# Kernel tuning notes

Measured on AMD Instinct MI355X. Metric: run time of the kernel, lower is better.

## Reference

```python
import jax, jax.numpy as jnp
import numpy as np

B, C, H, W = 32, 512, 64, 64
NBCLASS = 17


def setup_inputs() -> dict:
    key = jax.random.key(0)
    k1, k2 = jax.random.split(key, 2)
    x = jax.random.normal(k1, (B, C, H, W), dtype=jnp.float32)
    # 1x1 conv == linear over channels: weight (nbclass, C), bias (nbclass,)
    w_class = jax.random.normal(k2, (NBCLASS, C), dtype=jnp.float32) * 0.02
    b_class = jnp.zeros((NBCLASS,), dtype=jnp.float32)
    return {"x": x, "w_class": w_class, "b_class": b_class}


def reference(x, w_class, b_class):
    # x: (B, C, H, W); w_class: (K, C); b_class: (K,)
    Bx, Cx, Hx, Wx = x.shape
    # g = convclass(adaptive_avg_pool(x)) flattened -> (B, K)
    g = jnp.mean(x, axis=(2, 3)) @ w_class.T + b_class
    # cam = convclass(x) -> (B, K, H, W)
    cam = jnp.einsum('kc,bchw->bkhw', w_class, x) + b_class[None, :, None, None]
    # sf = mean_{h,w} sigmoid(cam)[:,k] * x[:,c]  -> (B, K, C)
    # (fused form of the original repeat/broadcast-multiply-mean)
    sf = jnp.einsum('bkhw,bchw->bkc', jax.nn.sigmoid(cam), x) / (Hx * Wx)
    return (g, sf)
```

## Files before the change

### kernel.cpp

```cpp
#include <hip/hip_runtime.h>
#include <cmath>

#define BATCH 32
#define CCH 512
#define HW 4096
#define KCL 17

typedef __attribute__((ext_vector_type(8))) short short8;
typedef __attribute__((ext_vector_type(16))) float f32x16;
typedef __attribute__((ext_vector_type(4))) float f32x4;

__device__ __forceinline__ unsigned pack_bf16(float a, float b) {
  unsigned ua = (__float_as_uint(a) + 0x8000u) >> 16;
  unsigned ub = (__float_as_uint(b) + 0x8000u) & 0xFFFF0000u;
  return ua | ub;
}
__device__ __forceinline__ f32x4 ntload4(const float* p) {
  return __builtin_nontemporal_load(reinterpret_cast<const f32x4*>(p));
}

#define WT_OFF 0
#define WT_BYTES (CCH * 20 * 4)
#define SIG_OFF WT_BYTES
#define SIG_BYTES ((size_t)BATCH * 32 * HW * 2)
#define XBF_OFF (SIG_OFF + SIG_BYTES)
#define XBF_BYTES ((size_t)BATCH * CCH * HW * 2)
#define WS_NEED (XBF_OFF + XBF_BYTES)

__global__ void k0_setup(const float* __restrict__ w, float* __restrict__ wT,
                         float* __restrict__ out_g) {
  int c = threadIdx.x;
  #pragma unroll
  for (int k = 0; k < 20; ++k) wT[c * 20 + k] = (k < KCL) ? w[k * CCH + c] : 0.f;
  if (c < BATCH * KCL) out_g[c] = 0.f;
  if (c < BATCH * KCL - 512) out_g[512 + c] = 0.f;
}

__global__ __launch_bounds__(512)
void k12_cam_sig(const float* __restrict__ x, const float* __restrict__ wT,
                 const float* __restrict__ bias, float* __restrict__ out_g,
                 unsigned short* __restrict__ xbf, unsigned short* __restrict__ sig) {
  extern __shared__ float R[];
  const int t = threadIdx.x;
  const int slab = __builtin_amdgcn_readfirstlane(t >> 7);
  const int pxg = t & 127;
  const int b = blockIdx.x >> 3;
  const int slice = blockIdx.x & 7;
  const int px = slice * 512 + pxg * 4;
  const float* xp = x + ((size_t)(b * CCH + slab * 128)) * HW + px;
  unsigned short* xbp = xbf + ((size_t)(b * CCH + slab * 128)) * HW + px;

  float cam[KCL][4];
  #pragma unroll
  for (int k = 0; k < KCL; ++k)
    #pragma unroll
    for (int i = 0; i < 4; ++i) cam[k][i] = 0.f;

  f32x4 v0[4], v1[4];
  #pragma unroll
  for (int j = 0; j < 4; ++j) v0[j] = ntload4(xp + (size_t)j * HW);

  #pragma unroll 1
  for (int gp = 0; gp < 16; ++gp) {
    const int c0 = gp * 8;
    #pragma unroll
    for (int j = 0; j < 4; ++j) v1[j] = ntload4(xp + (size_t)(c0 + 4 + j) * HW);
    #pragma unroll
    for (int j = 0; j < 4; ++j) {
      const f32x4 v = v0[j];
      const float* wr = wT + (slab * 128 + c0 + j) * 20;
      #pragma unroll
      for (int k = 0; k < KCL; ++k) {
        cam[k][0] = fmaf(wr[k], v.x, cam[k][0]);
        cam[k][1] = fmaf(wr[k], v.y, cam[k][1]);
        cam[k][2] = fmaf(wr[k], v.z, cam[k][2]);
        cam[k][3] = fmaf(wr[k], v.w, cam[k][3]);
      }
      *reinterpret_cast<uint2*>(xbp + (size_t)(c0 + j) * HW) =
          make_uint2(pack_bf16(v.x, v.y), pack_bf16(v.z, v.w));
    }
    if (gp < 15) {
      #pragma unroll
      for (int j = 0; j < 4; ++j) v0[j] = ntload4(xp + (size_t)(c0 + 8 + j) * HW);
    }
    #pragma unroll
    for (int j = 0; j < 4; ++j) {
      const f32x4 v = v1[j];
      const float* wr = wT + (slab * 128 + c0 + 4 + j) * 20;
      #pragma unroll
      for (int k = 0; k < KCL; ++k) {
        cam[k][0] = fmaf(wr[k], v.x, cam[k][0]);
        cam[k][1] = fmaf(wr[k], v.y, cam[k][1]);
        cam[k][2] = fmaf(wr[k], v.z, cam[k][2]);
        cam[k][3] = fmaf(wr[k], v.w, cam[k][3]);
      }
      *reinterpret_cast<uint2*>(xbp + (size_t)(c0 + 4 + j) * HW) =
          make_uint2(pack_bf16(v.x, v.y), pack_bf16(v.z, v.w));
    }
  }

  if (slab >= 2) {
    float* Rb = R + (slab - 2) * (KCL * 512);
    #pragma unroll
    for (int k = 0; k < KCL; ++k)
      *reinterpret_cast<float4*>(Rb + k * 512 + pxg * 4) =
          make_float4(cam[k][0], cam[k][1], cam[k][2], cam[k][3]);
  }
  __syncthreads();
  if (slab < 2) {
    const float* Rb = R + slab * (KCL * 512);
    #pragma unroll
    for (int k = 0; k < KCL; ++k) {
      const float4 r = *reinterpret_cast<const float4*>(Rb + k * 512 + pxg * 4);
      cam[k][0] += r.x; cam[k][1] += r.y; cam[k][2] += r.z; cam[k][3] += r.w;
    }
  }
  __syncthreads();
  if (slab == 1) {
    #pragma unroll
    for (int k = 0; k < KCL; ++k)
      *reinterpret_cast<float4*>(R + k * 512 + pxg * 4) =
          make_float4(cam[k][0], cam[k][1], cam[k][2], cam[k][3]);
  }
  __syncthreads();
  if (slab == 0) {
    const float inv = 1.f / 4096.f;
    const int lane = t & 63;
    #pragma unroll
    for (int k = 0; k < KCL; ++k) {
      const float4 r = *reinterpret_cast<const float4*>(R + k * 512 + pxg * 4);
      const float bk = bias[k];
      float c0 = cam[k][0] + r.x + bk;
      float c1 = cam[k][1] + r.y + bk;
      float c2 = cam[k][2] + r.z + bk;
      float c3 = cam[k][3] + r.w + bk;
      unsigned u0 = pack_bf16(1.f / (1.f + __expf(-c0)), 1.f / (1.f + __expf(-c1)));
      unsigned u1 = pack_bf16(1.f / (1.f + __expf(-c2)), 1.f / (1.f + __expf(-c3)));
      *reinterpret_cast<uint2*>(sig + ((size_t)(b * 32 + k)) * HW + px) = make_uint2(u0, u1);
      float gk = c0 + c1 + c2 + c3;
      #pragma unroll
      for (int o = 1; o < 64; o <<= 1) gk += __shfl_xor(gk, o, 64);
      if (lane == 0) atomicAdd(out_g + b * KCL + k, gk * inv);
    }
  }
}

__global__ __launch_bounds__(512, 2)
void k3_sf(const unsigned short* __restrict__ xbf, const unsigned short* __restrict__ sig,
           float* __restrict__ out_sf) {
  __shared__ float P[8 * 1024];
  const int p = blockIdx.x;
  const int lid = (p & 7) * 64 + (p >> 3);
  const int b = lid >> 4;
  const int chs = lid & 15;
  const int t = threadIdx.x;
  const int lane = t & 63;
  const int wv = __builtin_amdgcn_readfirstlane(t >> 6);
  const int m = lane & 31;
  const int h = lane >> 5;

  const unsigned short* ap = xbf + ((size_t)(b * CCH + chs * 32 + m)) * HW;
  const unsigned short* bp = sig + ((size_t)(b * 32 + m)) * HW;

  f32x16 acc;
  #pragma unroll
  for (int i = 0; i < 16; ++i) acc[i] = 0.f;

  const int obase = (wv * 64 + h) * 8;
  #pragma unroll 4
  for (int i = 0; i < 32; ++i) {
    const int o = obase + i * 16;
    const short8 a = *reinterpret_cast<const short8*>(ap + o);
    const short8 bb = *reinterpret_cast<const short8*>(bp + o);
    acc = __builtin_amdgcn_mfma_f32_32x32x16_bf16(a, bb, acc, 0, 0, 0);
  }

  #pragma unroll
  for (int r = 0; r < 16; ++r) {
    const int chr = (r & 3) + 8 * (r >> 2) + 4 * h;
    P[wv * 1024 + m * 32 + chr] = acc[r];
  }
  __syncthreads();
  const float inv = 1.f / 4096.f;
  {
    float s = 0.f;
    #pragma unroll
    for (int w8 = 0; w8 < 8; ++w8) s += P[w8 * 1024 + t];
    const int n = t >> 5, ch = t & 31;
    out_sf[((size_t)b * KCL + n) * CCH + chs * 32 + ch] = s * inv;
    if (t < 32) {
      float s2 = 0.f;
      #pragma unroll
      for (int w8 = 0; w8 < 8; ++w8) s2 += P[w8 * 1024 + 512 + t];
      out_sf[((size_t)b * KCL + 16) * CCH + chs * 32 + t] = s2 * inv;
    }
  }
}

extern "C" void kernel_launch(void* const* d_in, const int* in_sizes, int n_in,
                              void* d_out, int out_size, void* d_ws, size_t ws_size,
                              hipStream_t stream) {
  const float* x = (const float*)d_in[0];
  const float* w = (const float*)d_in[1];
  const float* bias = (const float*)d_in[2];
  float* out = (float*)d_out;
  float* outg = out;
  float* outsf = out + BATCH * KCL;

  char* ws = (char*)d_ws;
  float* wT = (float*)(ws + WT_OFF);
  unsigned short* sig = (unsigned short*)(ws + SIG_OFF);
  unsigned short* xbf = (unsigned short*)(ws + XBF_OFF);

  k0_setup<<<1, 512, 0, stream>>>(w, wT, outg);

  const int k12_lds = 2 * KCL * 512 * 4;
  hipFuncSetAttribute((const void*)k12_cam_sig,
                      hipFuncAttributeMaxDynamicSharedMemorySize, k12_lds);
  k12_cam_sig<<<BATCH * 8, 512, k12_lds, stream>>>(x, wT, bias, outg, xbf, sig);

  k3_sf<<<BATCH * 16, 512, 0, stream>>>(xbf, sig, outsf);
}
```

Baseline: 117.8 us.

## Split channels into eight slabs with eight pixels per thread in cam kernel

The cam/sigmoid kernel now gives each wave a 64-channel slab and has each thread cover 8 pixels instead of 4. Each weight load is reused across twice as many FMAs, and the bf16 stores widen to 16 bytes. The cross-slab reduction becomes a three-level tree through LDS, which is doubled to 4 slabs worth. The cost is twice the accumulator registers (136 floats), a 1-block-per-CU launch bound, and fewer memory loads in flight per thread relative to compute, which risks register pressure and lower occupancy.

```diff
diff --git a/kernel.cpp b/kernel.cpp
--- a/kernel.cpp
+++ b/kernel.cpp
@@ -27,6 +27,8 @@
 #define XBF_BYTES ((size_t)BATCH * CCH * HW * 2)
 #define WS_NEED (XBF_OFF + XBF_BYTES)
 
+#define K12_LDS (4 * KCL * 512 * 4)
+
 __global__ void k0_setup(const float* __restrict__ w, float* __restrict__ wT,
                          float* __restrict__ out_g) {
   int c = threadIdx.x;
@@ -36,111 +38,173 @@
   if (c < BATCH * KCL - 512) out_g[512 + c] = 0.f;
 }
 
-__global__ __launch_bounds__(512)
+__global__ __launch_bounds__(512, 1)
 void k12_cam_sig(const float* __restrict__ x, const float* __restrict__ wT,
                  const float* __restrict__ bias, float* __restrict__ out_g,
                  unsigned short* __restrict__ xbf, unsigned short* __restrict__ sig) {
   extern __shared__ float R[];
   const int t = threadIdx.x;
-  const int slab = __builtin_amdgcn_readfirstlane(t >> 7);
-  const int pxg = t & 127;
+  const int slab = __builtin_amdgcn_readfirstlane(t >> 6);
+  const int pxg = t & 63;
   const int b = blockIdx.x >> 3;
   const int slice = blockIdx.x & 7;
-  const int px = slice * 512 + pxg * 4;
-  const float* xp = x + ((size_t)(b * CCH + slab * 128)) * HW + px;
-  unsigned short* xbp = xbf + ((size_t)(b * CCH + slab * 128)) * HW + px;
-
-  float cam[KCL][4];
+  const int px = slice * 512 + pxg * 8;
+  const float* xp = x + ((size_t)(b * CCH + slab * 64)) * HW + px;
+  unsigned short* xbp = xbf + ((size_t)(b * CCH + slab * 64)) * HW + px;
+
+  float cam[KCL][8];
   #pragma unroll
   for (int k = 0; k < KCL; ++k)
     #pragma unroll
-    for (int i = 0; i < 4; ++i) cam[k][i] = 0.f;
-
-  f32x4 v0[4], v1[4];
-  #pragma unroll
-  for (int j = 0; j < 4; ++j) v0[j] = ntload4(xp + (size_t)j * HW);
+    for (int i = 0; i < 8; ++i) cam[k][i] = 0.f;
+
+  f32x4 v0[2][2], v1[2][2];
+  #pragma unroll
+  for (int j = 0; j < 2; ++j) {
+    v0[j][0] = ntload4(xp + (size_t)j * HW);
+    v0[j][1] = ntload4(xp + (size_t)j * HW + 4);
+  }
 
   #pragma unroll 1
   for (int gp = 0; gp < 16; ++gp) {
-    const int c0 = gp * 8;
-    #pragma unroll
-    for (int j = 0; j < 4; ++j) v1[j] = ntload4(xp + (size_t)(c0 + 4 + j) * HW);
-    #pragma unroll
-    for (int j = 0; j < 4; ++j) {
-      const f32x4 v = v0[j];
-      const float* wr = wT + (slab * 128 + c0 + j) * 20;
+    const int c0 = gp * 4;
+    #pragma unroll
+    for (int j = 0; j < 2; ++j) {
+      v1[j][0] = ntload4(xp + (size_t)(c0 + 2 + j) * HW);
+      v1[j][1] = ntload4(xp + (size_t)(c0 + 2 + j) * HW + 4);
+    }
+    #pragma unroll
+    for (int j = 0; j < 2; ++j) {
+      const f32x4 a = v0[j][0], q = v0[j][1];
+      const float* wr = wT + (slab * 64 + c0 + j) * 20;
       #pragma unroll
       for (int k = 0; k < KCL; ++k) {
-        cam[k][0] = fmaf(wr[k], v.x, cam[k][0]);
-        cam[k][1] = fmaf(wr[k], v.y, cam[k][1]);
-        cam[k][2] = fmaf(wr[k], v.z, cam[k][2]);
-        cam[k][3] = fmaf(wr[k], v.w, cam[k][3]);
+        const float wk = wr[k];
+        cam[k][0] = fmaf(wk, a.x, cam[k][0]);
+        cam[k][1] = fmaf(wk, a.y, cam[k][1]);
+        cam[k][2] = fmaf(wk, a.z, cam[k][2]);
+        cam[k][3] = fmaf(wk, a.w, cam[k][3]);
+        cam[k][4] = fmaf(wk, q.x, cam[k][4]);
+        cam[k][5] = fmaf(wk, q.y, cam[k][5]);
+        cam[k][6] = fmaf(wk, q.z, cam[k][6]);
+        cam[k][7] = fmaf(wk, q.w, cam[k][7]);
       }
-      *reinterpret_cast<uint2*>(xbp + (size_t)(c0 + j) * HW) =
-          make_uint2(pack_bf16(v.x, v.y), pack_bf16(v.z, v.w));
+      uint4 u;
+      u.x = pack_bf16(a.x, a.y);
+      u.y = pack_bf16(a.z, a.w);
+      u.z = pack_bf16(q.x, q.y);
+      u.w = pack_bf16(q.z, q.w);
+      *reinterpret_cast<uint4*>(xbp + (size_t)(c0 + j) * HW) = u;
     }
     if (gp < 15) {
       #pragma unroll
-      for (int j = 0; j < 4; ++j) v0[j] = ntload4(xp + (size_t)(c0 + 8 + j) * HW);
-    }
-    #pragma unroll
-    for (int j = 0; j < 4; ++j) {
-      const f32x4 v = v1[j];
-      const float* wr = wT + (slab * 128 + c0 + 4 + j) * 20;
+      for (int j = 0; j < 2; ++j) {
+        v0[j][0] = ntload4(xp + (size_t)(c0 + 4 + j) * HW);
+        v0[j][1] = ntload4(xp + (size_t)(c0 + 4 + j) * HW + 4);
+      }
+    }
+    #pragma unroll
+    for (int j = 0; j < 2; ++j) {
+      const f32x4 a = v1[j][0], q = v1[j][1];
+      const float* wr = wT + (slab * 64 + c0 + 2 + j) * 20;
       #pragma unroll
       for (int k = 0; k < KCL; ++k) {
-        cam[k][0] = fmaf(wr[k], v.x, cam[k][0]);
-        cam[k][1] = fmaf(wr[k], v.y, cam[k][1]);
-        cam[k][2] = fmaf(wr[k], v.z, cam[k][2]);
-        cam[k][3] = fmaf(wr[k], v.w, cam[k][3]);
+        const float wk = wr[k];
+        cam[k][0] = fmaf(wk, a.x, cam[k][0]);
+        cam[k][1] = fmaf(wk, a.y, cam[k][1]);
+        cam[k][2] = fmaf(wk, a.z, cam[k][2]);
+        cam[k][3] = fmaf(wk, a.w, cam[k][3]);
+        cam[k][4] = fmaf(wk, q.x, cam[k][4]);
+        cam[k][5] = fmaf(wk, q.y, cam[k][5]);
+        cam[k][6] = fmaf(wk, q.z, cam[k][6]);
+        cam[k][7] = fmaf(wk, q.w, cam[k][7]);
       }
-      *reinterpret_cast<uint2*>(xbp + (size_t)(c0 + 4 + j) * HW) =
-          make_uint2(pack_bf16(v.x, v.y), pack_bf16(v.z, v.w));
-    }
-  }
-
-  if (slab >= 2) {
+      uint4 u;
+      u.x = pack_bf16(a.x, a.y);
+      u.y = pack_bf16(a.z, a.w);
+      u.z = pack_bf16(q.x, q.y);
+      u.w = pack_bf16(q.z, q.w);
+      *reinterpret_cast<uint4*>(xbp + (size_t)(c0 + 2 + j) * HW) = u;
+    }
+  }
+
+  const int base = pxg * 8;
+  if (slab >= 4) {
+    float* Rb = R + (slab - 4) * (KCL * 512);
+    #pragma unroll
+    for (int k = 0; k < KCL; ++k) {
+      *reinterpret_cast<float4*>(Rb + k * 512 + base) =
+          make_float4(cam[k][0], cam[k][1], cam[k][2], cam[k][3]);
+      *reinterpret_cast<float4*>(Rb + k * 512 + base + 4) =
+          make_float4(cam[k][4], cam[k][5], cam[k][6], cam[k][7]);
+    }
+  }
+  __syncthreads();
+  if (slab < 4) {
+    const float* Rb = R + slab * (KCL * 512);
+    #pragma unroll
+    for (int k = 0; k < KCL; ++k) {
+      const float4 r0 = *reinterpret_cast<const float4*>(Rb + k * 512 + base);
+      const float4 r1 = *reinterpret_cast<const float4*>(Rb + k * 512 + base + 4);
+      cam[k][0] += r0.x; cam[k][1] += r0.y; cam[k][2] += r0.z; cam[k][3] += r0.w;
+      cam[k][4] += r1.x; cam[k][5] += r1.y; cam[k][6] += r1.z; cam[k][7] += r1.w;
+    }
+  }
+  __syncthreads();
+  if (slab == 2 || slab == 3) {
     float* Rb = R + (slab - 2) * (KCL * 512);
     #pragma unroll
-    for (int k = 0; k < KCL; ++k)
-      *reinterpret_cast<float4*>(Rb + k * 512 + pxg * 4) =
+    for (int k = 0; k < KCL; ++k) {
+      *reinterpret_cast<float4*>(Rb + k * 512 + base) =
           make_float4(cam[k][0], cam[k][1], cam[k][2], cam[k][3]);
+      *reinterpret_cast<float4*>(Rb + k * 512 + base + 4) =
+          make_float4(cam[k][4], cam[k][5], cam[k][6], cam[k][7]);
+    }
   }
   __syncthreads();
   if (slab < 2) {
     const float* Rb = R + slab * (KCL * 512);
     #pragma unroll
     for (int k = 0; k < KCL; ++k) {
-      const float4 r = *reinterpret_cast<const float4*>(Rb + k * 512 + pxg * 4);
-      cam[k][0] += r.x; cam[k][1] += r.y; cam[k][2] += r.z; cam[k][3] += r.w;
+      const float4 r0 = *reinterpret_cast<const float4*>(Rb + k * 512 + base);
+      const float4 r1 = *reinterpret_cast<const float4*>(Rb + k * 512 + base + 4);
+      cam[k][0] += r0.x; cam[k][1] += r0.y; cam[k][2] += r0.z; cam[k][3] += r0.w;
+      cam[k][4] += r1.x; cam[k][5] += r1.y; cam[k][6] += r1.z; cam[k][7] += r1.w;
     }
   }
   __syncthreads();
   if (slab == 1) {
     #pragma unroll
-    for (int k = 0; k < KCL; ++k)
-      *reinterpret_cast<float4*>(R + k * 512 + pxg * 4) =
+    for (int k = 0; k < KCL; ++k) {
+      *reinterpret_cast<float4*>(R + k * 512 + base) =
           make_float4(cam[k][0], cam[k][1], cam[k][2], cam[k][3]);
+      *reinterpret_cast<float4*>(R + k * 512 + base + 4) =
+          make_float4(cam[k][4], cam[k][5], cam[k][6], cam[k][7]);
+    }
   }
   __syncthreads();
   if (slab == 0) {
     const float inv = 1.f / 4096.f;
-    const int lane = t & 63;
-    #pragma unroll
-    for (int k = 0; k < KCL; ++k) {
-      const float4 r = *reinterpret_cast<const float4*>(R + k * 512 + pxg * 4);
+    #pragma unroll
+    for (int k = 0; k < KCL; ++k) {
+      const float4 r0 = *reinterpret_cast<const float4*>(R + k * 512 + base);
+      const float4 r1 = *reinterpret_cast<const float4*>(R + k * 512 + base + 4);
       const float bk = bias[k];
-      float c0 = cam[k][0] + r.x + bk;
-      float c1 = cam[k][1] + r.y + bk;
-      float c2 = cam[k][2] + r.z + bk;
-      float c3 = cam[k][3] + r.w + bk;
-      unsigned u0 = pack_bf16(1.f / (1.f + __expf(-c0)), 1.f / (1.f + __expf(-c1)));
-      unsigned u1 = pack_bf16(1.f / (1.f + __expf(-c2)), 1.f / (1.f + __expf(-c3)));
-      *reinterpret_cast<uint2*>(sig + ((size_t)(b * 32 + k)) * HW + px) = make_uint2(u0, u1);
-      float gk = c0 + c1 + c2 + c3;
+      float cf[8];
+      cf[0] = cam[k][0] + r0.x + bk; cf[1] = cam[k][1] + r0.y + bk;
+      cf[2] = cam[k][2] + r0.z + bk; cf[3] = cam[k][3] + r0.w + bk;
+      cf[4] = cam[k][4] + r1.x + bk; cf[5] = cam[k][5] + r1.y + bk;
+      cf[6] = cam[k][6] + r1.z + bk; cf[7] = cam[k][7] + r1.w + bk;
+      uint4 u;
+      u.x = pack_bf16(1.f / (1.f + __expf(-cf[0])), 1.f / (1.f + __expf(-cf[1])));
+      u.y = pack_bf16(1.f / (1.f + __expf(-cf[2])), 1.f / (1.f + __expf(-cf[3])));
+      u.z = pack_bf16(1.f / (1.f + __expf(-cf[4])), 1.f / (1.f + __expf(-cf[5])));
+      u.w = pack_bf16(1.f / (1.f + __expf(-cf[6])), 1.f / (1.f + __expf(-cf[7])));
+      *reinterpret_cast<uint4*>(sig + ((size_t)(b * 32 + k)) * HW + px) = u;
+      float gk = cf[0] + cf[1] + cf[2] + cf[3] + cf[4] + cf[5] + cf[6] + cf[7];
       #pragma unroll
       for (int o = 1; o < 64; o <<= 1) gk += __shfl_xor(gk, o, 64);
-      if (lane == 0) atomicAdd(out_g + b * KCL + k, gk * inv);
+      if ((t & 63) == 0) atomicAdd(out_g + b * KCL + k, gk * inv);
     }
   }
 }
@@ -214,10 +278,9 @@
 
   k0_setup<<<1, 512, 0, stream>>>(w, wT, outg);
 
-  const int k12_lds = 2 * KCL * 512 * 4;
   hipFuncSetAttribute((const void*)k12_cam_sig,
-                      hipFuncAttributeMaxDynamicSharedMemorySize, k12_lds);
-  k12_cam_sig<<<BATCH * 8, 512, k12_lds, stream>>>(x, wT, bias, outg, xbf, sig);
+                      hipFuncAttributeMaxDynamicSharedMemorySize, K12_LDS);
+  k12_cam_sig<<<BATCH * 8, 512, K12_LDS, stream>>>(x, wT, bias, outg, xbf, sig);
 
   k3_sf<<<BATCH * 16, 512, 0, stream>>>(xbf, sig, outsf);
 }
```

Result: slower. 128.2 us (+8.8%).
